# Kernel tuning notes

Measured on AMD Instinct MI355X. Metric: run time of the kernel, lower is better.

Reference implementation:

```python
import jax, jax.numpy as jnp
import numpy as np

B, S, H, NH, HD = 2, 2048, 1024, 16, 64
THETA = 10000.0


def setup_inputs() -> dict:
    key = jax.random.key(0)
    k1, k2, k3, k4, k5 = jax.random.split(key, 5)
    hidden_states = jax.random.normal(k1, (B, S, H), dtype=jnp.float32)
    # RoPE tables, interleaved-pair layout: [c0,c0,c1,c1,...] along head_dim
    inv_freq = 1.0 / (THETA ** (jnp.arange(0, HD, 2, dtype=jnp.float32) / HD))
    t = jnp.arange(S, dtype=jnp.float32)
    freqs = jnp.outer(t, inv_freq)                      # [S, HD//2]
    freqs_cos = jnp.repeat(jnp.cos(freqs), 2, axis=-1)  # [S, HD]
    freqs_sin = jnp.repeat(jnp.sin(freqs), 2, axis=-1)  # [S, HD]
    position_ids = jnp.arange(S, dtype=jnp.int32)
    w = 0.02
    Wq = jax.random.normal(k2, (H, H), dtype=jnp.float32) * w
    Wk = jax.random.normal(k3, (H, H), dtype=jnp.float32) * w
    Wv = jax.random.normal(k4, (H, H), dtype=jnp.float32) * w
    Wo = jax.random.normal(k5, (H, H), dtype=jnp.float32) * w
    return {"hidden_states": hidden_states, "freqs_cos": freqs_cos,
            "freqs_sin": freqs_sin, "position_ids": position_ids,
            "Wq": Wq, "Wk": Wk, "Wv": Wv, "Wo": Wo}


def _rotate_half_interleaved(x):
    # stack([-x[..., 1::2], x[..., ::2]], -1).reshape_as(x)
    xe = x.reshape(x.shape[:-1] + (HD // 2, 2))
    return jnp.stack([-xe[..., 1], xe[..., 0]], axis=-1).reshape(x.shape)


def reference(hidden_states, freqs_cos, freqs_sin, position_ids, Wq, Wk, Wv, Wo):
    b, s, _ = hidden_states.shape
    # QKV projections (torch Linear: y = x @ W.T), split into heads [b, nh, s, hd]
    q = jnp.einsum('bsh,oh->bso', hidden_states, Wq).reshape(b, s, NH, HD).transpose(0, 2, 1, 3)
    k = jnp.einsum('bsh,oh->bso', hidden_states, Wk).reshape(b, s, NH, HD).transpose(0, 2, 1, 3)
    v = jnp.einsum('bsh,oh->bso', hidden_states, Wv).reshape(b, s, NH, HD).transpose(0, 2, 1, 3)
    cos = freqs_cos[position_ids][None, None]  # [1, 1, s, hd]
    sin = freqs_sin[position_ids][None, None]
    rq = _rotate_half_interleaved(q)
    # NOTE: faithful to source bug — rotate_half_k is built from q, not k
    q = q * cos + rq * sin
    k = k * cos + rq * sin
    # causal SDPA, scale = 1/sqrt(head_dim)
    scores = jnp.einsum('bhqd,bhkd->bhqk', q, k) / jnp.sqrt(jnp.float32(HD))
    causal = jnp.tril(jnp.ones((s, s), dtype=bool))
    scores = jnp.where(causal, scores, jnp.float32(-1e30))
    attn = jax.nn.softmax(scores, axis=-1)
    out = jnp.einsum('bhqk,bhkd->bhqd', attn, v)
    out = out.transpose(0, 2, 1, 3).reshape(b, s, H)
    return jnp.einsum('bsh,oh->bso', out, Wo)
```

## Files before the change

### kernel.cpp

```cpp
#include <hip/hip_runtime.h>
#include <stdint.h>

#define BB 2
#define SS 2048
#define HH 1024
#define NHH 16
#define HDD 64

typedef short bf16s;
typedef __attribute__((ext_vector_type(8))) short short8;
typedef __attribute__((ext_vector_type(4))) short short4v;
typedef __attribute__((ext_vector_type(2))) short short2v;
typedef __attribute__((ext_vector_type(4))) float f32x4;
typedef _Float16 half4v __attribute__((ext_vector_type(4)));
typedef _Float16 half8v __attribute__((ext_vector_type(8)));
typedef __fp16 fp16x2 __attribute__((ext_vector_type(2)));

__device__ inline short f2bf(float f) {
  union { float f; uint32_t u; } v; v.f = f;
  uint32_t r = (v.u + 0x7fffu + ((v.u >> 16) & 1u)) >> 16;
  return (short)r;
}
__device__ inline float bf2f(short h) {
  union { uint32_t u; float f; } v; v.u = ((uint32_t)(uint16_t)h) << 16;
  return v.f;
}

__device__ __forceinline__ float exp2_raw(float x) {
  float r;
  asm("v_exp_f32 %0, %1\n\ts_nop 0" : "=v"(r) : "v"(x));
  return r;
}

__device__ inline void gld_lds16(const void* g, void* l) {
  __builtin_amdgcn_global_load_lds((const __attribute__((address_space(1))) void*)g,
                                   (__attribute__((address_space(3))) void*)l, 16, 0, 0);
}

__device__ inline void stv(short* C, size_t i, float v) { C[i] = f2bf(v); }
__device__ inline void stv(float* C, size_t i, float v) { C[i] = v; }

__global__ __launch_bounds__(256) void convert_all(
    const float* __restrict__ x, const float* __restrict__ Wq,
    const float* __restrict__ Wk, const float* __restrict__ Wv,
    const float* __restrict__ Wo, bf16s* __restrict__ xb,
    bf16s* __restrict__ wqkv, bf16s* __restrict__ wob) {
  const long M1 = 1024L * 1024L;
  long e = (long)(blockIdx.x * blockDim.x + threadIdx.x) * 4;
  const float* src; bf16s* dst;
  if (e < 4 * M1)      { src = x  + e;            dst = xb   + e; }
  else if (e < 5 * M1) { src = Wq + (e - 4 * M1); dst = wqkv + (e - 4 * M1); }
  else if (e < 6 * M1) { src = Wk + (e - 5 * M1); dst = wqkv + (e - 4 * M1); }
  else if (e < 7 * M1) { src = Wv + (e - 6 * M1); dst = wqkv + (e - 4 * M1); }
  else                 { src = Wo + (e - 7 * M1); dst = wob  + (e - 7 * M1); }
  float4 v = *(const float4*)src;
  short4v o;
  o.x = f2bf(v.x); o.y = f2bf(v.y); o.z = f2bf(v.z); o.w = f2bf(v.w);
  *(short4v*)dst = o;
}

template <typename OT>
__global__ __launch_bounds__(256) void gemm_bt(
    const bf16s* __restrict__ A, const bf16s* __restrict__ Bm,
    OT* __restrict__ C, int K, int ldc) {
  __shared__ __align__(16) bf16s As[128 * 64];
  __shared__ __align__(16) bf16s Bs[128 * 64];
  const int tid = threadIdx.x;
  const int lane = tid & 63, w = tid >> 6;
  const int quad = lane >> 4, mcol = lane & 15;
  const int bm = blockIdx.y * 128, bn = blockIdx.x * 128;
  const int wm = (w >> 1) * 64, wn = (w & 1) * 64;
  f32x4 acc[4][4] = {};
  const int nkt = K >> 6;
  for (int kt = 0; kt < nkt; ++kt) {
    __syncthreads();
#pragma unroll
    for (int i = 0; i < 4; ++i) {
      int seg = (i * 4 + w) * 512;
      int flat = seg + lane * 8;
      int row = flat >> 6;
      int cpos = (flat >> 3) & 7;
      int cs = cpos ^ (row & 7);
      gld_lds16(A + (size_t)(bm + row) * K + kt * 64 + cs * 8, &As[seg]);
      gld_lds16(Bm + (size_t)(bn + row) * K + kt * 64 + cs * 8, &Bs[seg]);
    }
    __syncthreads();
#pragma unroll
    for (int ks = 0; ks < 2; ++ks) {
      short8 af[4], bf[4];
#pragma unroll
      for (int mt = 0; mt < 4; ++mt) {
        int row = wm + mt * 16 + mcol;
        int cs = (ks * 4 + quad) ^ (row & 7);
        af[mt] = *(const short8*)&As[row * 64 + cs * 8];
      }
#pragma unroll
      for (int nt = 0; nt < 4; ++nt) {
        int row = wn + nt * 16 + mcol;
        int cs = (ks * 4 + quad) ^ (row & 7);
        bf[nt] = *(const short8*)&Bs[row * 64 + cs * 8];
      }
#pragma unroll
      for (int mt = 0; mt < 4; ++mt)
#pragma unroll
        for (int nt = 0; nt < 4; ++nt)
          acc[mt][nt] = __builtin_amdgcn_mfma_f32_16x16x32_bf16(af[mt], bf[nt], acc[mt][nt], 0, 0, 0);
    }
  }
#pragma unroll
  for (int mt = 0; mt < 4; ++mt)
#pragma unroll
    for (int nt = 0; nt < 4; ++nt) {
      int r0 = bm + wm + mt * 16 + quad * 4;
      int c = bn + wn + nt * 16 + mcol;
#pragma unroll
      for (int r = 0; r < 4; ++r)
        stv(C, (size_t)(r0 + r) * ldc + c, acc[mt][nt][r]);
    }
}

__global__ __launch_bounds__(256) void rope_qk(
    const bf16s* __restrict__ qkv, const float* __restrict__ fcos,
    const float* __restrict__ fsin, const int* __restrict__ pos,
    bf16s* __restrict__ Q, bf16s* __restrict__ Kc) {
  const float LOG2E = 1.4426950408889634f;
  int t = blockIdx.x * blockDim.x + threadIdx.x;
  int i = t & 31;
  int h = (t >> 5) & 15;
  int m = t >> 9;
  int s = m & 2047, b = m >> 11;
  int p = pos[s];
  float c = fcos[p * 64 + 2 * i];
  float sn = fsin[p * 64 + 2 * i];
  const bf16s* qp = qkv + (size_t)m * 3072 + h * 64 + 2 * i;
  float q0 = bf2f(qp[0]), q1 = bf2f(qp[1]);
  float k0 = bf2f(qp[1024]), k1 = bf2f(qp[1025]);
  float rq0 = -q1, rq1 = q0;
  size_t o = ((size_t)(b * 16 + h) * 2048 + s) * 64 + 2 * i;
  short2v qo, ko;
  qo.x = f2bf((q0 * c + rq0 * sn) * 0.125f);
  qo.y = f2bf((q1 * c + rq1 * sn) * 0.125f);
  ko.x = f2bf((k0 * c + rq0 * sn) * LOG2E);
  ko.y = f2bf((k1 * c + rq1 * sn) * LOG2E);
  *(short2v*)&Q[o] = qo;
  *(short2v*)&Kc[o] = ko;
}

__global__ __launch_bounds__(256) void transpose_v(
    const bf16s* __restrict__ qkv, _Float16* __restrict__ Vt) {
  __shared__ __align__(16) _Float16 T[64 * 72];
  int st = blockIdx.x, bh = blockIdx.y;
  int b = bh >> 4, h = bh & 15;
  int tid = threadIdx.x;
  int m0 = b * 2048 + st * 64;
#pragma unroll
  for (int p2 = 0; p2 < 2; ++p2) {
    int sl = p2 * 32 + (tid >> 3);
    int ch = tid & 7;
    short8 v = *(const short8*)&qkv[(size_t)(m0 + sl) * 3072 + 2048 + h * 64 + ch * 8];
#pragma unroll
    for (int j = 0; j < 8; ++j) T[(ch * 8 + j) * 72 + sl] = (_Float16)bf2f(v[j]);
  }
  __syncthreads();
#pragma unroll
  for (int p2 = 0; p2 < 2; ++p2) {
    int dl = p2 * 32 + (tid >> 3);
    int ch = tid & 7;
    half8v v = *(const half8v*)&T[dl * 72 + ch * 8];
    *(half8v*)&Vt[((size_t)bh * 64 + dl) * 2048 + st * 64 + ch * 8] = v;
  }
}

template <bool DOB>
__device__ __forceinline__ void step2(
    const bf16s* __restrict__ Ks, const _Float16* __restrict__ Vs,
    const short8* bqA, const short8* bqB,
    f32x4* OA, f32x4* OB, float& lA, float& lB,
    bool diagA, bool diagB, int w, int quad, int col) {
  f32x4 sA[4], sB[4];
#pragma unroll
  for (int t = 0; t < 4; ++t) {
    f32x4 a = {}, bb = {};
#pragma unroll
    for (int ks = 0; ks < 2; ++ks) {
      int krow = t * 16 + col;
      int cs = (ks * 4 + quad) ^ (krow & 7);
      short8 af = *(const short8*)&Ks[krow * 64 + cs * 8];
      a = __builtin_amdgcn_mfma_f32_16x16x32_bf16(af, bqA[ks], a, 0, 0, 0);
      if (DOB) bb = __builtin_amdgcn_mfma_f32_16x16x32_bf16(af, bqB[ks], bb, 0, 0, 0);
    }
    sA[t] = a;
    if (DOB) sB[t] = bb;
  }
  if (diagA) {
#pragma unroll
    for (int t = 0; t < 4; ++t)
#pragma unroll
      for (int r = 0; r < 4; ++r)
        if (t * 16 + quad * 4 + r > w * 16 + col) sA[t][r] = -1e30f;
  }
  if (DOB && diagB) {
#pragma unroll
    for (int t = 0; t < 4; ++t)
#pragma unroll
      for (int r = 0; r < 4; ++r)
        if (t * 16 + quad * 4 + r > w * 16 + col) sB[t][r] = -1e30f;
  }
  half4v paA[4], paB[4];
#pragma unroll
  for (int t = 0; t < 4; ++t) {
    {
      float p0 = exp2_raw(sA[t][0]), p1 = exp2_raw(sA[t][1]);
      float p2 = exp2_raw(sA[t][2]), p3 = exp2_raw(sA[t][3]);
      lA += (p0 + p1) + (p2 + p3);
      union { fp16x2 h2[2]; half4v h4; } u;
      u.h2[0] = __builtin_amdgcn_cvt_pkrtz(p0, p1);
      u.h2[1] = __builtin_amdgcn_cvt_pkrtz(p2, p3);
      paA[t] = u.h4;
    }
    if (DOB) {
      float p0 = exp2_raw(sB[t][0]), p1 = exp2_raw(sB[t][1]);
      float p2 = exp2_raw(sB[t][2]), p3 = exp2_raw(sB[t][3]);
      lB += (p0 + p1) + (p2 + p3);
      union { fp16x2 h2[2]; half4v h4; } u;
      u.h2[0] = __builtin_amdgcn_cvt_pkrtz(p0, p1);
      u.h2[1] = __builtin_amdgcn_cvt_pkrtz(p2, p3);
      paB[t] = u.h4;
    }
  }
#pragma unroll
  for (int t = 0; t < 4; ++t)
#pragma unroll
    for (int dt = 0; dt < 4; ++dt) {
      int vrow = dt * 16 + col;
      half4v bv = *(const half4v*)&Vs[vrow * 68 + t * 16 + quad * 4];
      OA[dt] = __builtin_amdgcn_mfma_f32_16x16x16f16(paA[t], bv, OA[dt], 0, 0, 0);
      if (DOB) OB[dt] = __builtin_amdgcn_mfma_f32_16x16x16f16(paB[t], bv, OB[dt], 0, 0, 0);
    }
}

__global__ __launch_bounds__(256) void attn(
    const bf16s* __restrict__ Q, const bf16s* __restrict__ Kb,
    const _Float16* __restrict__ Vt, bf16s* __restrict__ O) {
  __shared__ __align__(16) bf16s Ks[64 * 64];
  __shared__ __align__(16) _Float16 Vs[64 * 68];
  const int bh = blockIdx.y;
  const int tid = threadIdx.x, lane = tid & 63, w = tid >> 6;
  const int quad = lane >> 4, col = lane & 15;
  const size_t base = (size_t)bh * 2048 * 64;
  const _Float16* vbase = Vt + (size_t)bh * 64 * 2048;
  const int b = bh >> 4, h = bh & 15;
  const int x = blockIdx.x;
  const int qbA = 31 - x, qbB = x;

  short8 bqA[2], bqB[2];
  {
    const int qrA = qbA * 64 + w * 16 + col;
    const int qrB = qbB * 64 + w * 16 + col;
#pragma unroll
    for (int ks = 0; ks < 2; ++ks) {
      bqA[ks] = *(const short8*)&Q[base + (size_t)qrA * 64 + ks * 32 + quad * 8];
      bqB[ks] = *(const short8*)&Q[base + (size_t)qrB * 64 + ks * 32 + quad * 8];
    }
  }
  f32x4 OA[4] = {}, OB[4] = {};
  float lA = 0.f, lB = 0.f;

  const int vd = tid >> 2, vc = tid & 3;
  for (int kt = 0; kt <= qbA; ++kt) {
    half8v vreg0 = *(const half8v*)&vbase[(size_t)vd * 2048 + kt * 64 + vc * 16];
    half8v vreg1 = *(const half8v*)&vbase[(size_t)vd * 2048 + kt * 64 + vc * 16 + 8];
    __syncthreads();
    *(half8v*)&Vs[vd * 68 + vc * 16] = vreg0;
    *(half8v*)&Vs[vd * 68 + vc * 16 + 8] = vreg1;
#pragma unroll
    for (int i = 0; i < 2; ++i) {
      int seg = (i * 4 + w) * 512;
      int flat = seg + lane * 8;
      int row = flat >> 6, cpos = (flat >> 3) & 7;
      int cs = cpos ^ (row & 7);
      gld_lds16(&Kb[base + (size_t)(kt * 64 + row) * 64 + cs * 8], &Ks[seg]);
    }
    __syncthreads();
    if (kt <= qbB)
      step2<true>(Ks, Vs, bqA, bqB, OA, OB, lA, lB,
                  false, kt == qbB, w, quad, col);
    else
      step2<false>(Ks, Vs, bqA, bqB, OA, OB, lA, lB,
                   kt == qbA, false, w, quad, col);
  }

  lA += __shfl_xor(lA, 16); lA += __shfl_xor(lA, 32);
  lB += __shfl_xor(lB, 16); lB += __shfl_xor(lB, 32);

#pragma unroll
  for (int which = 0; which < 2; ++which) {
    const int qb = which ? qbB : qbA;
    const f32x4* Oacc = which ? OB : OA;
    const float l = which ? lB : lA;
    float l4[4];
#pragma unroll
    for (int r = 0; r < 4; ++r) l4[r] = __shfl(l, quad * 4 + r);
#pragma unroll
    for (int dt = 0; dt < 4; ++dt)
#pragma unroll
      for (int r = 0; r < 4; ++r) {
        int srow = qb * 64 + w * 16 + quad * 4 + r;
        O[((size_t)b * 2048 + srow) * 1024 + h * 64 + dt * 16 + col] =
            f2bf(Oacc[dt][r] / l4[r]);
      }
  }
}

extern "C" void kernel_launch(void* const* d_in, const int* in_sizes, int n_in,
                              void* d_out, int out_size, void* d_ws, size_t ws_size,
                              hipStream_t stream) {
  (void)in_sizes; (void)n_in; (void)out_size; (void)ws_size;
  const float* x  = (const float*)d_in[0];
  const float* fc = (const float*)d_in[1];
  const float* fs = (const float*)d_in[2];
  const int* pos  = (const int*)d_in[3];
  const float* Wq = (const float*)d_in[4];
  const float* Wk = (const float*)d_in[5];
  const float* Wv = (const float*)d_in[6];
  const float* Wo = (const float*)d_in[7];
  float* out = (float*)d_out;
  char* ws = (char*)d_ws;
  const size_t MB = 1024 * 1024;
  bf16s* xb   = (bf16s*)(ws);
  bf16s* wqkv = (bf16s*)(ws + 8 * MB);
  bf16s* wob  = (bf16s*)(ws + 14 * MB);
  bf16s* qkv  = (bf16s*)(ws + 16 * MB);
  bf16s* Qb   = (bf16s*)(ws + 40 * MB);
  bf16s* Kb   = (bf16s*)(ws + 48 * MB);
  _Float16* Vt = (_Float16*)(ws + 56 * MB);
  bf16s* Ob   = (bf16s*)(ws);

  convert_all<<<8192, 256, 0, stream>>>(x, Wq, Wk, Wv, Wo, xb, wqkv, wob);
  gemm_bt<bf16s><<<dim3(24, 32), 256, 0, stream>>>(xb, wqkv, qkv, 1024, 3072);
  rope_qk<<<8192, 256, 0, stream>>>(qkv, fc, fs, pos, Qb, Kb);
  transpose_v<<<dim3(32, 32), 256, 0, stream>>>(qkv, Vt);
  attn<<<dim3(16, 32), 256, 0, stream>>>(Qb, Kb, Vt, Ob);
  gemm_bt<float><<<dim3(8, 32), 256, 0, stream>>>(Ob, wob, out, 1024, 1024);
}
```

Measured before the change: 193.6 us.

## Fuse RoPE with V transpose, swizzle V LDS, fp16 output GEMM with smaller M tile

Merges the rope_qk and transpose_v kernels into one postproc kernel with vectorized 16-element loads per thread, removing a launch and improving memory access width. In attention, the V tile in LDS is stored with an XOR-rotated layout so each lane reads 8-wide vectors instead of scattered 4-wide reads, aiming to cut bank conflicts and LDS instruction count. The attention output and Wo are switched to fp16, using the f16 MFMA in the output projection. That GEMM is templated to a 64-row M tile, doubling its grid to fill more CUs. The fp16 change alters rounding behaviour slightly.

New measurement: 191.3 us. No clear change (-1.2%).

```diff
diff --git a/kernel.cpp b/kernel.cpp
--- a/kernel.cpp
+++ b/kernel.cpp
@@ -40,40 +40,67 @@
 __device__ inline void stv(short* C, size_t i, float v) { C[i] = f2bf(v); }
 __device__ inline void stv(float* C, size_t i, float v) { C[i] = v; }
 
+__device__ inline f32x4 mfma_k32(short8 a, short8 b, f32x4 c) {
+  return __builtin_amdgcn_mfma_f32_16x16x32_bf16(a, b, c, 0, 0, 0);
+}
+__device__ inline f32x4 mfma_k32(half8v a, half8v b, f32x4 c) {
+  return __builtin_amdgcn_mfma_f32_16x16x32_f16(a, b, c, 0, 0, 0);
+}
+template <typename ET> struct ftr;
+template <> struct ftr<short>     { using v8 = short8; };
+template <> struct ftr<_Float16>  { using v8 = half8v; };
+
 __global__ __launch_bounds__(256) void convert_all(
     const float* __restrict__ x, const float* __restrict__ Wq,
     const float* __restrict__ Wk, const float* __restrict__ Wv,
     const float* __restrict__ Wo, bf16s* __restrict__ xb,
-    bf16s* __restrict__ wqkv, bf16s* __restrict__ wob) {
+    bf16s* __restrict__ wqkv, _Float16* __restrict__ wof) {
   const long M1 = 1024L * 1024L;
   long e = (long)(blockIdx.x * blockDim.x + threadIdx.x) * 4;
-  const float* src; bf16s* dst;
-  if (e < 4 * M1)      { src = x  + e;            dst = xb   + e; }
-  else if (e < 5 * M1) { src = Wq + (e - 4 * M1); dst = wqkv + (e - 4 * M1); }
-  else if (e < 6 * M1) { src = Wk + (e - 5 * M1); dst = wqkv + (e - 4 * M1); }
-  else if (e < 7 * M1) { src = Wv + (e - 6 * M1); dst = wqkv + (e - 4 * M1); }
-  else                 { src = Wo + (e - 7 * M1); dst = wob  + (e - 7 * M1); }
-  float4 v = *(const float4*)src;
-  short4v o;
-  o.x = f2bf(v.x); o.y = f2bf(v.y); o.z = f2bf(v.z); o.w = f2bf(v.w);
-  *(short4v*)dst = o;
-}
-
-template <typename OT>
+  if (e < 7 * M1) {
+    const float* src; bf16s* dst;
+    if (e < 4 * M1)      { src = x  + e;            dst = xb   + e; }
+    else if (e < 5 * M1) { src = Wq + (e - 4 * M1); dst = wqkv + (e - 4 * M1); }
+    else if (e < 6 * M1) { src = Wk + (e - 5 * M1); dst = wqkv + (e - 4 * M1); }
+    else                 { src = Wv + (e - 6 * M1); dst = wqkv + (e - 4 * M1); }
+    float4 v = *(const float4*)src;
+    short4v o;
+    o.x = f2bf(v.x); o.y = f2bf(v.y); o.z = f2bf(v.z); o.w = f2bf(v.w);
+    *(short4v*)dst = o;
+  } else {
+    float4 v = *(const float4*)(Wo + (e - 7 * M1));
+    half4v o;
+    o.x = (_Float16)v.x; o.y = (_Float16)v.y;
+    o.z = (_Float16)v.z; o.w = (_Float16)v.w;
+    *(half4v*)(wof + (e - 7 * M1)) = o;
+  }
+}
+
+template <typename ET, typename OT, int MT>
 __global__ __launch_bounds__(256) void gemm_bt(
-    const bf16s* __restrict__ A, const bf16s* __restrict__ Bm,
+    const ET* __restrict__ A, const ET* __restrict__ Bm,
     OT* __restrict__ C, int K, int ldc) {
-  __shared__ __align__(16) bf16s As[128 * 64];
-  __shared__ __align__(16) bf16s Bs[128 * 64];
+  using V8 = typename ftr<ET>::v8;
+  __shared__ __align__(16) ET As[MT * 32 * 64];
+  __shared__ __align__(16) ET Bs[128 * 64];
   const int tid = threadIdx.x;
   const int lane = tid & 63, w = tid >> 6;
   const int quad = lane >> 4, mcol = lane & 15;
-  const int bm = blockIdx.y * 128, bn = blockIdx.x * 128;
-  const int wm = (w >> 1) * 64, wn = (w & 1) * 64;
-  f32x4 acc[4][4] = {};
+  const int bm = blockIdx.y * (MT * 32), bn = blockIdx.x * 128;
+  const int wm = (w >> 1) * (MT * 16), wn = (w & 1) * 64;
+  f32x4 acc[MT][4] = {};
   const int nkt = K >> 6;
   for (int kt = 0; kt < nkt; ++kt) {
     __syncthreads();
+#pragma unroll
+    for (int i = 0; i < MT; ++i) {
+      int seg = (i * 4 + w) * 512;
+      int flat = seg + lane * 8;
+      int row = flat >> 6;
+      int cpos = (flat >> 3) & 7;
+      int cs = cpos ^ (row & 7);
+      gld_lds16(A + (size_t)(bm + row) * K + kt * 64 + cs * 8, &As[seg]);
+    }
 #pragma unroll
     for (int i = 0; i < 4; ++i) {
       int seg = (i * 4 + w) * 512;
@@ -81,34 +108,33 @@
       int row = flat >> 6;
       int cpos = (flat >> 3) & 7;
       int cs = cpos ^ (row & 7);
-      gld_lds16(A + (size_t)(bm + row) * K + kt * 64 + cs * 8, &As[seg]);
       gld_lds16(Bm + (size_t)(bn + row) * K + kt * 64 + cs * 8, &Bs[seg]);
     }
     __syncthreads();
 #pragma unroll
     for (int ks = 0; ks < 2; ++ks) {
-      short8 af[4], bf[4];
-#pragma unroll
-      for (int mt = 0; mt < 4; ++mt) {
+      V8 af[MT], bf[4];
+#pragma unroll
+      for (int mt = 0; mt < MT; ++mt) {
         int row = wm + mt * 16 + mcol;
         int cs = (ks * 4 + quad) ^ (row & 7);
-        af[mt] = *(const short8*)&As[row * 64 + cs * 8];
+        af[mt] = *(const V8*)&As[row * 64 + cs * 8];
       }
 #pragma unroll
       for (int nt = 0; nt < 4; ++nt) {
         int row = wn + nt * 16 + mcol;
         int cs = (ks * 4 + quad) ^ (row & 7);
-        bf[nt] = *(const short8*)&Bs[row * 64 + cs * 8];
+        bf[nt] = *(const V8*)&Bs[row * 64 + cs * 8];
       }
 #pragma unroll
-      for (int mt = 0; mt < 4; ++mt)
+      for (int mt = 0; mt < MT; ++mt)
 #pragma unroll
         for (int nt = 0; nt < 4; ++nt)
-          acc[mt][nt] = __builtin_amdgcn_mfma_f32_16x16x32_bf16(af[mt], bf[nt], acc[mt][nt], 0, 0, 0);
-    }
-  }
-#pragma unroll
-  for (int mt = 0; mt < 4; ++mt)
+          acc[mt][nt] = mfma_k32(af[mt], bf[nt], acc[mt][nt]);
+    }
+  }
+#pragma unroll
+  for (int mt = 0; mt < MT; ++mt)
 #pragma unroll
     for (int nt = 0; nt < 4; ++nt) {
       int r0 = bm + wm + mt * 16 + quad * 4;
@@ -119,40 +145,42 @@
     }
 }
 
-__global__ __launch_bounds__(256) void rope_qk(
+__global__ __launch_bounds__(256) void postproc(
     const bf16s* __restrict__ qkv, const float* __restrict__ fcos,
     const float* __restrict__ fsin, const int* __restrict__ pos,
-    bf16s* __restrict__ Q, bf16s* __restrict__ Kc) {
+    bf16s* __restrict__ Q, bf16s* __restrict__ Kc, _Float16* __restrict__ Vt) {
   const float LOG2E = 1.4426950408889634f;
-  int t = blockIdx.x * blockDim.x + threadIdx.x;
-  int i = t & 31;
-  int h = (t >> 5) & 15;
-  int m = t >> 9;
-  int s = m & 2047, b = m >> 11;
-  int p = pos[s];
-  float c = fcos[p * 64 + 2 * i];
-  float sn = fsin[p * 64 + 2 * i];
-  const bf16s* qp = qkv + (size_t)m * 3072 + h * 64 + 2 * i;
-  float q0 = bf2f(qp[0]), q1 = bf2f(qp[1]);
-  float k0 = bf2f(qp[1024]), k1 = bf2f(qp[1025]);
-  float rq0 = -q1, rq1 = q0;
-  size_t o = ((size_t)(b * 16 + h) * 2048 + s) * 64 + 2 * i;
-  short2v qo, ko;
-  qo.x = f2bf((q0 * c + rq0 * sn) * 0.125f);
-  qo.y = f2bf((q1 * c + rq1 * sn) * 0.125f);
-  ko.x = f2bf((k0 * c + rq0 * sn) * LOG2E);
-  ko.y = f2bf((k1 * c + rq1 * sn) * LOG2E);
-  *(short2v*)&Q[o] = qo;
-  *(short2v*)&Kc[o] = ko;
-}
-
-__global__ __launch_bounds__(256) void transpose_v(
-    const bf16s* __restrict__ qkv, _Float16* __restrict__ Vt) {
+  const int st = blockIdx.x, bh = blockIdx.y;
+  const int b = bh >> 4, h = bh & 15;
+  const int tid = threadIdx.x;
+  const int m0 = b * 2048 + st * 64;
+  {
+    const int row = tid >> 2, pc = tid & 3;
+    const int s = st * 64 + row;
+    const int p = pos[s];
+    const bf16s* qp = qkv + (size_t)(m0 + row) * 3072 + h * 64 + pc * 16;
+    short8 qv[2] = { *(const short8*)qp, *(const short8*)(qp + 8) };
+    short8 kv[2] = { *(const short8*)(qp + 1024), *(const short8*)(qp + 1032) };
+    const float* cp = fcos + (size_t)p * 64 + pc * 16;
+    const float* sp = fsin + (size_t)p * 64 + pc * 16;
+    short8 qo[2], ko[2];
+#pragma unroll
+    for (int hf = 0; hf < 2; ++hf)
+#pragma unroll
+      for (int j = 0; j < 4; ++j) {
+        float c = cp[hf * 8 + 2 * j], sn = sp[hf * 8 + 2 * j];
+        float q0 = bf2f(qv[hf][2 * j]), q1 = bf2f(qv[hf][2 * j + 1]);
+        float k0 = bf2f(kv[hf][2 * j]), k1 = bf2f(kv[hf][2 * j + 1]);
+        qo[hf][2 * j]     = f2bf((q0 * c - q1 * sn) * 0.125f);
+        qo[hf][2 * j + 1] = f2bf((q1 * c + q0 * sn) * 0.125f);
+        ko[hf][2 * j]     = f2bf((k0 * c - q1 * sn) * LOG2E);
+        ko[hf][2 * j + 1] = f2bf((k1 * c + q0 * sn) * LOG2E);
+      }
+    size_t o = ((size_t)bh * 2048 + s) * 64 + pc * 16;
+    *(short8*)&Q[o] = qo[0];  *(short8*)&Q[o + 8] = qo[1];
+    *(short8*)&Kc[o] = ko[0]; *(short8*)&Kc[o + 8] = ko[1];
+  }
   __shared__ __align__(16) _Float16 T[64 * 72];
-  int st = blockIdx.x, bh = blockIdx.y;
-  int b = bh >> 4, h = bh & 15;
-  int tid = threadIdx.x;
-  int m0 = b * 2048 + st * 64;
 #pragma unroll
   for (int p2 = 0; p2 < 2; ++p2) {
     int sl = p2 * 32 + (tid >> 3);
@@ -173,7 +201,7 @@
 
 template <bool DOB>
 __device__ __forceinline__ void step2(
-    const bf16s* __restrict__ Ks, const _Float16* __restrict__ Vs,
+    const bf16s* __restrict__ Ks, const _Float16* __restrict__ Vp,
     const short8* bqA, const short8* bqB,
     f32x4* OA, f32x4* OB, float& lA, float& lB,
     bool diagA, bool diagB, int w, int quad, int col) {
@@ -229,21 +257,26 @@
     }
   }
 #pragma unroll
-  for (int t = 0; t < 4; ++t)
-#pragma unroll
-    for (int dt = 0; dt < 4; ++dt) {
-      int vrow = dt * 16 + col;
-      half4v bv = *(const half4v*)&Vs[vrow * 68 + t * 16 + quad * 4];
-      OA[dt] = __builtin_amdgcn_mfma_f32_16x16x16f16(paA[t], bv, OA[dt], 0, 0, 0);
-      if (DOB) OB[dt] = __builtin_amdgcn_mfma_f32_16x16x16f16(paB[t], bv, OB[dt], 0, 0, 0);
-    }
+  for (int dt = 0; dt < 4; ++dt) {
+    int vrow = dt * 16 + col;
+    const _Float16* vp = &Vp[vrow * 72 + (quad ^ (vrow & 3)) * 16];
+    union { half8v v8; half4v v4[2]; } a01, a23;
+    a01.v8 = *(const half8v*)vp;
+    a23.v8 = *(const half8v*)(vp + 8);
+    half4v bv[4] = { a01.v4[0], a01.v4[1], a23.v4[0], a23.v4[1] };
+#pragma unroll
+    for (int t = 0; t < 4; ++t) {
+      OA[dt] = __builtin_amdgcn_mfma_f32_16x16x16f16(paA[t], bv[t], OA[dt], 0, 0, 0);
+      if (DOB) OB[dt] = __builtin_amdgcn_mfma_f32_16x16x16f16(paB[t], bv[t], OB[dt], 0, 0, 0);
+    }
+  }
 }
 
 __global__ __launch_bounds__(256) void attn(
     const bf16s* __restrict__ Q, const bf16s* __restrict__ Kb,
-    const _Float16* __restrict__ Vt, bf16s* __restrict__ O) {
+    const _Float16* __restrict__ Vt, _Float16* __restrict__ O) {
   __shared__ __align__(16) bf16s Ks[64 * 64];
-  __shared__ __align__(16) _Float16 Vs[64 * 68];
+  __shared__ __align__(16) _Float16 Vp[64 * 72];
   const int bh = blockIdx.y;
   const int tid = threadIdx.x, lane = tid & 63, w = tid >> 6;
   const int quad = lane >> 4, col = lane & 15;
@@ -267,12 +300,20 @@
   float lA = 0.f, lB = 0.f;
 
   const int vd = tid >> 2, vc = tid & 3;
+  const int rot = vd & 3;
   for (int kt = 0; kt <= qbA; ++kt) {
-    half8v vreg0 = *(const half8v*)&vbase[(size_t)vd * 2048 + kt * 64 + vc * 16];
-    half8v vreg1 = *(const half8v*)&vbase[(size_t)vd * 2048 + kt * 64 + vc * 16 + 8];
+    half8v vr0 = *(const half8v*)&vbase[(size_t)vd * 2048 + kt * 64 + vc * 16];
+    half8v vr1 = *(const half8v*)&vbase[(size_t)vd * 2048 + kt * 64 + vc * 16 + 8];
     __syncthreads();
-    *(half8v*)&Vs[vd * 68 + vc * 16] = vreg0;
-    *(half8v*)&Vs[vd * 68 + vc * 16 + 8] = vreg1;
+    {
+      union { half8v v8; half4v v4[2]; } u0, u1;
+      u0.v8 = vr0; u1.v8 = vr1;
+      int rbase = vd * 72 + vc * 4;
+      *(half4v*)&Vp[rbase + (0 ^ rot) * 16] = u0.v4[0];
+      *(half4v*)&Vp[rbase + (1 ^ rot) * 16] = u0.v4[1];
+      *(half4v*)&Vp[rbase + (2 ^ rot) * 16] = u1.v4[0];
+      *(half4v*)&Vp[rbase + (3 ^ rot) * 16] = u1.v4[1];
+    }
 #pragma unroll
     for (int i = 0; i < 2; ++i) {
       int seg = (i * 4 + w) * 512;
@@ -283,10 +324,10 @@
     }
     __syncthreads();
     if (kt <= qbB)
-      step2<true>(Ks, Vs, bqA, bqB, OA, OB, lA, lB,
+      step2<true>(Ks, Vp, bqA, bqB, OA, OB, lA, lB,
                   false, kt == qbB, w, quad, col);
     else
-      step2<false>(Ks, Vs, bqA, bqB, OA, OB, lA, lB,
+      step2<false>(Ks, Vp, bqA, bqB, OA, OB, lA, lB,
                    kt == qbA, false, w, quad, col);
   }
 
@@ -307,7 +348,7 @@
       for (int r = 0; r < 4; ++r) {
         int srow = qb * 64 + w * 16 + quad * 4 + r;
         O[((size_t)b * 2048 + srow) * 1024 + h * 64 + dt * 16 + col] =
-            f2bf(Oacc[dt][r] / l4[r]);
+            (_Float16)(Oacc[dt][r] / l4[r]);
       }
   }
 }
@@ -327,19 +368,18 @@
   float* out = (float*)d_out;
   char* ws = (char*)d_ws;
   const size_t MB = 1024 * 1024;
-  bf16s* xb   = (bf16s*)(ws);
-  bf16s* wqkv = (bf16s*)(ws + 8 * MB);
-  bf16s* wob  = (bf16s*)(ws + 14 * MB);
-  bf16s* qkv  = (bf16s*)(ws + 16 * MB);
-  bf16s* Qb   = (bf16s*)(ws + 40 * MB);
-  bf16s* Kb   = (bf16s*)(ws + 48 * MB);
+  bf16s* xb    = (bf16s*)(ws);
+  bf16s* wqkv  = (bf16s*)(ws + 8 * MB);
+  _Float16* wof = (_Float16*)(ws + 14 * MB);
+  bf16s* qkv   = (bf16s*)(ws + 16 * MB);
+  bf16s* Qb    = (bf16s*)(ws + 40 * MB);
+  bf16s* Kb    = (bf16s*)(ws + 48 * MB);
   _Float16* Vt = (_Float16*)(ws + 56 * MB);
-  bf16s* Ob   = (bf16s*)(ws);
-
-  convert_all<<<8192, 256, 0, stream>>>(x, Wq, Wk, Wv, Wo, xb, wqkv, wob);
-  gemm_bt<bf16s><<<dim3(24, 32), 256, 0, stream>>>(xb, wqkv, qkv, 1024, 3072);
-  rope_qk<<<8192, 256, 0, stream>>>(qkv, fc, fs, pos, Qb, Kb);
-  transpose_v<<<dim3(32, 32), 256, 0, stream>>>(qkv, Vt);
+  _Float16* Ob = (_Float16*)(ws);
+
+  convert_all<<<8192, 256, 0, stream>>>(x, Wq, Wk, Wv, Wo, xb, wqkv, wof);
+  gemm_bt<short, short, 4><<<dim3(24, 32), 256, 0, stream>>>(xb, wqkv, qkv, 1024, 3072);
+  postproc<<<dim3(32, 32), 256, 0, stream>>>(qkv, fc, fs, pos, Qb, Kb, Vt);
   attn<<<dim3(16, 32), 256, 0, stream>>>(Qb, Kb, Vt, Ob);
-  gemm_bt<float><<<dim3(8, 32), 256, 0, stream>>>(Ob, wob, out, 1024, 1024);
-}
+  gemm_bt<_Float16, float, 2><<<dim3(8, 64), 256, 0, stream>>>(Ob, wof, out, 1024, 1024);
+}
```
